# Kernel tuning notes

Measured on AMD Instinct MI355X. Metric: run time of the kernel, lower is better.

Reference implementation:

```python
import jax, jax.numpy as jnp
import numpy as np
import math

B, L, D, H = 4, 1024, 768, 12   # docs, seq_len, hidden, attn heads
E, M, P = 24, 4, 552            # entities/doc, mentions/entity, pairs/doc
EMB, BLK, NL = 768, 64, 97      # emb_size, block_size, num relation labels


def setup_inputs() -> dict:
    key = jax.random.key(0)
    ks = jax.random.split(key, 12)
    s = 0.02  # weight init scale
    return {
        "sequence_output": jax.random.normal(ks[0], (B, L, D), jnp.float32),
        "attention": jax.random.uniform(ks[1], (B, H, L, L), jnp.float32),
        "W_q": jax.random.normal(ks[2], (D, D), jnp.float32) * s,
        "W_k": jax.random.normal(ks[3], (D, D), jnp.float32) * s,
        "head_W": jax.random.normal(ks[4], (2 * D, EMB), jnp.float32) * s,
        "head_b": jax.random.normal(ks[5], (EMB,), jnp.float32) * s,
        "tail_W": jax.random.normal(ks[6], (2 * D, EMB), jnp.float32) * s,
        "tail_b": jax.random.normal(ks[7], (EMB,), jnp.float32) * s,
        "bil_W": jax.random.normal(ks[8], (EMB * BLK, NL), jnp.float32) * s,
        "bil_b": jax.random.normal(ks[9], (NL,), jnp.float32) * s,
        "mention_pos": jax.random.randint(ks[10], (B, E, M), 0, L - 2),
        "hts": jax.random.randint(ks[11], (B, P, 2), 0, E),
    }


def reference(sequence_output, attention, W_q, W_k, head_W, head_b,
              tail_W, tail_b, bil_W, bil_b, mention_pos, hts):
    offset = 1  # bert-style [CLS] offset
    pos = mention_pos + offset                     # [B,E,M] token index of each mention
    bb = jnp.arange(B)[:, None, None]

    # --- mention gathers (padded version of the ragged python loops) ---
    # per-mention attention rows: attention[b, :, pos, :] -> [B,E,M,H,L]
    att_q = attention.transpose(0, 2, 1, 3)        # [B,L,H,L]
    ment_att = att_q[bb, pos]                      # [B,E,M,H,L]
    ent_att = ment_att.mean(axis=2)                # [B,E,H,L]  (mean over mentions)
    # mention embeddings (GAT stage = identity here): [B,E,M,D]
    ment_emb = sequence_output[bb, pos]

    # --- localized context rs via head*tail attention product ---
    bb2 = jnp.arange(B)[:, None]
    h_att = ent_att[bb2, hts[:, :, 0]]             # [B,P,H,L]
    t_att = ent_att[bb2, hts[:, :, 1]]             # [B,P,H,L]
    ht_att = (h_att * t_att).mean(axis=2)          # [B,P,L] (mean over heads)
    ht_att = ht_att / (ht_att.sum(axis=-1, keepdims=True) + 1e-5)
    rs = jnp.einsum('bld,bpl->bpd', sequence_output, ht_att)  # [B,P,D]

    R = B * P
    rs_f = rs.reshape(R, D)

    # --- entity representations via mention-level attention pooling ---
    h_ment = ment_emb[bb2, hts[:, :, 0]].reshape(R, M, D)
    t_ment = ment_emb[bb2, hts[:, :, 1]].reshape(R, M, D)
    q_c = rs_f @ W_q                               # [R,D]
    inv = 1.0 / math.sqrt(D)

    def pool(ment):
        k = ment.reshape(-1, D) @ W_k
        k = k.reshape(R, M, D)
        scores = jnp.einsum('rmd,rd->rm', k, q_c) * inv
        w = jax.nn.softmax(scores, axis=-1)
        return jnp.einsum('rm,rmd->rd', w, ment)

    h_ent = pool(h_ment)                           # [R,D]
    t_ent = pool(t_ment)                           # [R,D]

    # --- extractors + grouped bilinear classifier ---
    hs = jnp.tanh(jnp.concatenate([h_ent, rs_f], axis=1) @ head_W + head_b)
    ts = jnp.tanh(jnp.concatenate([t_ent, rs_f], axis=1) @ tail_W + tail_b)
    K = EMB // BLK
    b1 = hs.reshape(R, K, BLK)
    b2 = ts.reshape(R, K, BLK)
    bl = (b1[:, :, :, None] * b2[:, :, None, :]).reshape(R, EMB * BLK)
    logits = bl @ bil_W + bil_b                    # [R,NL]
    return logits
```

## Files before the change

### kernel.cpp

```cpp
#include <hip/hip_runtime.h>
#include <hip/hip_bf16.h>
#include <math.h>

#define Bc 4
#define Lc 1024
#define Dc 768
#define Hc 12
#define Ec 24
#define Mc 4
#define Pc 552
#define EMBc 768
#define NLc 97
#define Rc (Bc*Pc)
#define KSPL 48
#define HT_ABS (35*32*512)

typedef __attribute__((ext_vector_type(4))) float f32x4;
typedef __attribute__((ext_vector_type(8))) short short8;
typedef __attribute__((ext_vector_type(4))) unsigned short us4;
typedef _Float16 f16x8 __attribute__((ext_vector_type(8)));

static __device__ __forceinline__ unsigned short f2bf(float x){
  unsigned int u = __float_as_uint(x);
  unsigned int r = u + 0x7fffu + ((u >> 16) & 1u);
  return (unsigned short)(r >> 16);
}
static __device__ __forceinline__ unsigned short f2h(float x){
  _Float16 h = (_Float16)x;
  return __builtin_bit_cast(unsigned short, h);
}
static __device__ __forceinline__ float h2f(unsigned short x){
  return (float)__builtin_bit_cast(_Float16, x);
}
static __device__ __forceinline__ size_t flin_off(int r, int kk, int KT){
  return ((size_t)(r>>4)*KT + (kk>>5))*512 + (size_t)((((kk&31)>>3)*16 + (r&15))*8) + (kk&7);
}

__global__ __launch_bounds__(256) void k_prep(const float* __restrict__ bilW, unsigned short* __restrict__ Wbf,
                                              const float* __restrict__ seq, unsigned short* __restrict__ seqf,
                                              const float* __restrict__ W_q, unsigned short* __restrict__ Wq_f,
                                              const float* __restrict__ W_k, unsigned short* __restrict__ Wk_f,
                                              const float* __restrict__ headW, unsigned short* __restrict__ headW_f,
                                              const float* __restrict__ tailW, unsigned short* __restrict__ tailW_f,
                                              const float* __restrict__ att, const int* __restrict__ mpos,
                                              float* __restrict__ ent_att,
                                              unsigned short* __restrict__ ment_bf){
  int bx = blockIdx.x;
  int tid = threadIdx.x;
  __shared__ float t[64][65];
  if (bx < 1536){
    const float* Ws = bilW + (size_t)bx*32*NLc;
    unsigned short* o = Wbf + (size_t)bx*4480;
    float* w = &t[0][0];
    for (int idx = tid; idx < 32*NLc; idx += 256)
      w[idx] = Ws[idx];
    __syncthreads();
    #pragma unroll
    for (int q8 = 0; q8 < 18; q8++){
      int idx = q8*256 + tid;
      if (idx < 4480){
        int n = idx / 40, kk = idx - n*40;
        float v = (kk < 32 && n < NLc) ? w[kk*NLc + n] : 0.f;
        o[idx] = f2h(v);
      }
    }
    return;
  }
  if (bx >= 3168){
    int blk = bx - 3168;
    int h  = blk % Hc;
    int be = blk / Hc;
    int b  = be / Ec;
    int p0 = mpos[be*Mc+0]+1, p1 = mpos[be*Mc+1]+1;
    int p2 = mpos[be*Mc+2]+1, p3 = mpos[be*Mc+3]+1;
    const float* ab = att + ((size_t)b*Hc + h)*Lc*Lc;
    const float* a0 = ab + (size_t)p0*Lc;
    const float* a1 = ab + (size_t)p1*Lc;
    const float* a2 = ab + (size_t)p2*Lc;
    const float* a3 = ab + (size_t)p3*Lc;
    float* o = ent_att + (size_t)blk*Lc;
    int l4 = tid*4;
    float4 v0 = *(const float4*)(a0 + l4);
    float4 v1 = *(const float4*)(a1 + l4);
    float4 v2 = *(const float4*)(a2 + l4);
    float4 v3 = *(const float4*)(a3 + l4);
    float4 ov;
    ov.x = 0.25f*(v0.x+v1.x+v2.x+v3.x);
    ov.y = 0.25f*(v0.y+v1.y+v2.y+v3.y);
    ov.z = 0.25f*(v0.z+v1.z+v2.z+v3.z);
    ov.w = 0.25f*(v0.w+v1.w+v2.w+v3.w);
    *(float4*)(o + l4) = ov;
    int gidx = blk*256 + tid;
    int d = gidx % Dc;
    int bem = gidx / Dc;
    int bb = bem / (Ec*Mc);
    int pos = mpos[bem] + 1;
    float v = seq[((size_t)bb*Lc + pos)*Dc + d];
    ment_bf[flin_off(bem, d, 24)] = f2bf(v);
    return;
  }
  bx -= 1536;
  const float* src; unsigned short* dst; int tk, tn, KTW;
  if (bx < 768){
    int z = bx / 192, rem = bx % 192;
    src = seq + (size_t)z*Lc*Dc; dst = seqf + (size_t)z*(Dc/16)*(Lc/32)*512;
    tk = rem % 16; tn = rem / 16; KTW = 32;
  } else if (bx < 768+144){
    int rem = bx - 768;
    src = W_q; dst = Wq_f; tk = rem % 12; tn = rem / 12; KTW = 24;
  } else if (bx < 768+288){
    int rem = bx - (768+144);
    src = W_k; dst = Wk_f; tk = rem % 12; tn = rem / 12; KTW = 24;
  } else if (bx < 768+288+288){
    int rem = bx - (768+288);
    src = headW; dst = headW_f; tk = rem % 24; tn = rem / 24; KTW = 48;
  } else {
    int rem = bx - (768+288+288);
    src = tailW; dst = tailW_f; tk = rem % 24; tn = rem / 24; KTW = 48;
  }
  int r0 = tk*64, c0 = tn*64;
  #pragma unroll
  for (int q8 = 0; q8 < 16; q8++){
    int idx = q8*256 + tid;
    int rr = idx >> 6, cc = idx & 63;
    t[rr][cc] = src[(size_t)(r0+rr)*768 + c0+cc];
  }
  __syncthreads();
  #pragma unroll
  for (int q8 = 0; q8 < 16; q8++){
    int idx = q8*256 + tid;
    int li = idx & 511, sub = idx >> 9;
    int nt_l = sub >> 1, kt_l = sub & 1;
    int lane = li >> 3, e = li & 7;
    int kl = kt_l*32 + (lane>>4)*8 + e;
    int nl = nt_l*16 + (lane&15);
    dst[ ((size_t)(c0/16 + nt_l)*KTW + (r0/32 + kt_l))*512 + li ] = f2bf(t[kl][nl]);
  }
}

__global__ __launch_bounds__(256) void k_ht_att(const float* __restrict__ ent_att,
                                                const int* __restrict__ hts,
                                                unsigned short* __restrict__ htbf){
  int b = blockIdx.x & 3;
  int p = blockIdx.x >> 2;
  unsigned short* o = htbf + (size_t)b*HT_ABS;
  int l4 = threadIdx.x*4;
  if (p >= Pc){
    us4 z4 = {0,0,0,0};
    *(us4*)(o + flin_off(p, l4, 32)) = z4;
    return;
  }
  int r = b*Pc + p;
  int hi = hts[r*2+0], ti = hts[r*2+1];
  const float* eh = ent_att + (size_t)(b*Ec+hi)*Hc*Lc;
  const float* et = ent_att + (size_t)(b*Ec+ti)*Hc*Lc;
  __shared__ float raw[Lc];
  __shared__ float wsum[4];
  float4 s4 = {0.f,0.f,0.f,0.f};
  #pragma unroll
  for (int h = 0; h < Hc; h++){
    float4 e1 = *(const float4*)&eh[h*Lc + l4];
    float4 e2 = *(const float4*)&et[h*Lc + l4];
    s4.x = fmaf(e1.x,e2.x,s4.x); s4.y = fmaf(e1.y,e2.y,s4.y);
    s4.z = fmaf(e1.z,e2.z,s4.z); s4.w = fmaf(e1.w,e2.w,s4.w);
  }
  s4.x *= (1.0f/Hc); s4.y *= (1.0f/Hc); s4.z *= (1.0f/Hc); s4.w *= (1.0f/Hc);
  *(float4*)&raw[l4] = s4;
  float lsum = s4.x+s4.y+s4.z+s4.w;
  for (int off = 32; off; off >>= 1) lsum += __shfl_down(lsum, off);
  if ((threadIdx.x & 63) == 0) wsum[threadIdx.x>>6] = lsum;
  __syncthreads();
  float inv = 1.0f/(wsum[0]+wsum[1]+wsum[2]+wsum[3] + 1e-5f);
  float4 rv = *(const float4*)&raw[l4];
  us4 v4;
  v4[0] = f2bf(rv.x*inv); v4[1] = f2bf(rv.y*inv);
  v4[2] = f2bf(rv.z*inv); v4[3] = f2bf(rv.w*inv);
  *(us4*)(o + flin_off(p, l4, 32)) = v4;
}

struct FJob {
  const unsigned short* A1; const unsigned short* W; const float* bias; void* C;
  int M; int mtmax; int Wktw; int rowsPerBatch;
  size_t Abs; size_t Wbs;
};
struct FJobs {
  FJob j[6]; int xs[7]; int n;
};

template<int KT1, int CT, int NT>
__global__ __launch_bounds__(256) void k_fgemmN(FJobs P){
  int tid = threadIdx.x;
  int jx = 0;
  for (int tjob = 1; tjob < P.n; tjob++)
    if ((int)blockIdx.x >= P.xs[tjob]) jx = tjob;
  FJob j = P.j[jx];
  int mbx = blockIdx.x - P.xs[jx];
  int z = blockIdx.z;
  int lane = tid & 63, wid = tid >> 6;
  int row16 = lane & 15, oct = lane >> 4;

  __shared__ __align__(16) unsigned short Wlds[NT*KT1*512];
  {
    const unsigned short* wpan = j.W + (size_t)z*j.Wbs + (size_t)(blockIdx.y*NT)*j.Wktw*512;
    constexpr int UNITS = NT*KT1*64;
    #pragma unroll
    for (int it = 0; it < UNITS/256; ++it){
      int u = it*256 + tid;
      int f = u >> 6;
      int n = f / KT1, kt = f - n*KT1;
      size_t so = (((size_t)(n*j.Wktw + kt)) << 9) + (size_t)((u & 63) << 3);
      __builtin_amdgcn_global_load_lds(
          (const __attribute__((address_space(1))) unsigned int*)(wpan + so),
          (__attribute__((address_space(3))) unsigned int*)((char*)Wlds + (size_t)u*16),
          16, 0, 0);
    }
  }

  int rb = mbx*128 + wid*32;
  int mt0 = rb >> 4;       if (mt0 >= j.mtmax) mt0 = j.mtmax - 1;
  int mt1 = (rb >> 4) + 1; if (mt1 >= j.mtmax) mt1 = j.mtmax - 1;
  const unsigned short* ap0 = j.A1 + (size_t)z*j.Abs + (size_t)mt0*KT1*512 + lane*8;
  const unsigned short* ap1 = j.A1 + (size_t)z*j.Abs + (size_t)mt1*KT1*512 + lane*8;
  f32x4 acc[2][NT];
  #pragma unroll
  for (int m = 0; m < 2; m++)
    #pragma unroll
    for (int n = 0; n < NT; n++) acc[m][n] = (f32x4){0.f,0.f,0.f,0.f};

  __syncthreads();

  #pragma unroll 4
  for (int kt = 0; kt < KT1; kt++){
    short8 a0 = *(const short8*)(ap0 + (size_t)kt*512);
    short8 a1 = *(const short8*)(ap1 + (size_t)kt*512);
    #pragma unroll
    for (int n = 0; n < NT; n++){
      short8 bv = *(const short8*)&Wlds[(n*KT1 + kt)*512 + lane*8];
      acc[0][n] = __builtin_amdgcn_mfma_f32_16x16x32_bf16(a0, bv, acc[0][n], 0, 0, 0);
      acc[1][n] = __builtin_amdgcn_mfma_f32_16x16x32_bf16(a1, bv, acc[1][n], 0, 0, 0);
    }
  }
  int colb = blockIdx.y*(NT*16);
  #pragma unroll
  for (int m = 0; m < 2; m++)
    #pragma unroll
    for (int n = 0; n < NT; n++)
      #pragma unroll
      for (int jj = 0; jj < 4; jj++){
        int r = rb + m*16 + oct*4 + jj;
        if (r < j.M){
          int col = colb + n*16 + row16;
          float v = acc[m][n][jj];
          if (CT == 0 && j.bias) v += j.bias[col];
          int rg = z*j.rowsPerBatch + r;
          if (CT == 2){
            ((unsigned short*)j.C)[flin_off(rg, col, 24)] = f2bf(v);
          } else {
            ((float*)j.C)[(size_t)rg*768 + col] = v;
          }
        }
      }
}

__global__ __launch_bounds__(256) void k_pool(const float* __restrict__ kment,
                                              const float* __restrict__ q_c,
                                              const float* __restrict__ rsWh,
                                              const float* __restrict__ rsWt,
                                              const float* __restrict__ mWh,
                                              const float* __restrict__ mWt,
                                              const float* __restrict__ headb,
                                              const float* __restrict__ tailb,
                                              const int* __restrict__ hts,
                                              unsigned short* __restrict__ hs16,
                                              unsigned short* __restrict__ ts16){
  int wid = threadIdx.x >> 6, lane = threadIdx.x & 63;
  int r = blockIdx.x*4 + wid;
  int b = r / Pc;
  float q[12];
  const float* qp = q_c + (size_t)r*Dc + lane;
  #pragma unroll
  for (int u = 0; u < 12; u++) q[u] = qp[u*64];
  const float invs = 0.03608439182435161f;
  #pragma unroll
  for (int side = 0; side < 2; side++){
    int e = hts[r*2+side];
    const float* kb = kment + (size_t)(b*Ec+e)*Mc*Dc + lane;
    float part[Mc] = {0.f,0.f,0.f,0.f};
    #pragma unroll
    for (int m = 0; m < Mc; m++)
      #pragma unroll
      for (int u = 0; u < 12; u++)
        part[m] = fmaf(kb[m*Dc + u*64], q[u], part[m]);
    #pragma unroll
    for (int m = 0; m < Mc; m++)
      #pragma unroll
      for (int off = 1; off < 64; off <<= 1)
        part[m] += __shfl_xor(part[m], off);
    float mx = fmaxf(fmaxf(part[0],part[1]), fmaxf(part[2],part[3])) * invs;
    float w0 = expf(part[0]*invs - mx), w1 = expf(part[1]*invs - mx);
    float w2 = expf(part[2]*invs - mx), w3 = expf(part[3]*invs - mx);
    float isum = 1.0f/(w0+w1+w2+w3);
    w0 *= isum; w1 *= isum; w2 *= isum; w3 *= isum;
    const float* mW  = (side ? mWt  : mWh) + (size_t)(b*Ec+e)*Mc*Dc;
    const float* rsW = (side ? rsWt : rsWh) + (size_t)r*Dc;
    const float* bias = side ? tailb : headb;
    unsigned short* o = (side ? ts16 : hs16) + (size_t)r*Dc;
    #pragma unroll
    for (int u = 0; u < 12; u++){
      int d = lane + u*64;
      float v = rsW[d] + bias[d]
              + w0*mW[d] + w1*mW[Dc+d] + w2*mW[2*Dc+d] + w3*mW[3*Dc+d];
      o[d] = f2h(tanhf(v));
    }
  }
}

__global__ __launch_bounds__(256) void k_bilinear_mfma(
    const unsigned short* __restrict__ hs16, const unsigned short* __restrict__ ts16,
    const unsigned short* __restrict__ Wbf,
    unsigned short* __restrict__ partial)
{
  int mb = blockIdx.x / KSPL;
  int kb = blockIdx.x % KSPL;
  int k  = kb >> 2;
  int i0 = (kb & 3) * 16;

  int tid  = threadIdx.x;
  int lane = tid & 63;
  int wid  = tid >> 6;
  int row16 = lane & 15;
  int oct   = lane >> 4;

  int rbase = mb*256 + wid*64;

  __shared__ __align__(16) unsigned short Wlds[2][8960];

  f16x8 tsh[4][2];
  f16x8 hsh[4][2];
  #pragma unroll
  for (int m = 0; m < 4; m++){
    int r = rbase + m*16 + row16; if (r > Rc-1) r = Rc-1;
    const unsigned short* tp = ts16 + (size_t)r*EMBc + k*64;
    tsh[m][0] = __builtin_bit_cast(f16x8, *(const short8*)(tp + oct*8));
    tsh[m][1] = __builtin_bit_cast(f16x8, *(const short8*)(tp + 32 + oct*8));
    const unsigned short* hp = hs16 + (size_t)r*EMBc + k*64 + i0;
    hsh[m][0] = __builtin_bit_cast(f16x8, *(const short8*)(hp));
    hsh[m][1] = __builtin_bit_cast(f16x8, *(const short8*)(hp + 8));
  }

  const char* wsrc = (const char*)(Wbf + ((size_t)(k*128 + i0*2))*4480);

  #pragma unroll
  for (int rr = 0; rr < 5; rr++){
    int u = tid + rr*256;
    if (u < 1120)
      __builtin_amdgcn_global_load_lds(
        (const __attribute__((address_space(1))) unsigned int*)(wsrc + (size_t)u*16),
        (__attribute__((address_space(3))) unsigned int*)((char*)&Wlds[0][0] + u*16),
        16, 0, 0);
  }

  f32x4 acc[4][7];
  #pragma unroll
  for (int m = 0; m < 4; m++)
    #pragma unroll
    for (int n = 0; n < 7; n++) acc[m][n] = (f32x4){0.f,0.f,0.f,0.f};

  __syncthreads();

  #pragma unroll
  for (int cp = 0; cp < 16; cp++){
    int cur = cp & 1;
    if (cp < 15){
      const char* nsrc = wsrc + (size_t)(cp+1)*17920;
      #pragma unroll
      for (int rr = 0; rr < 5; rr++){
        int u = tid + rr*256;
        if (u < 1120)
          __builtin_amdgcn_global_load_lds(
            (const __attribute__((address_space(1))) unsigned int*)(nsrc + (size_t)u*16),
            (__attribute__((address_space(3))) unsigned int*)((char*)&Wlds[cur^1][0] + u*16),
            16, 0, 0);
      }
    }
    #pragma unroll
    for (int half = 0; half < 2; half++){
      f16x8 af[4];
      #pragma unroll
      for (int m = 0; m < 4; m++){
        _Float16 hv = hsh[m][cp>>3][cp&7];
        f16x8 hvb = {hv,hv,hv,hv,hv,hv,hv,hv};
        af[m] = tsh[m][half] * hvb;
      }
      #pragma unroll
      for (int n = 0; n < 7; n++){
        f16x8 bfr = __builtin_bit_cast(f16x8,
            *(const short8*)&Wlds[cur][half*4480 + (n*16 + row16)*40 + oct*8]);
        #pragma unroll
        for (int m = 0; m < 4; m++)
          acc[m][n] = __builtin_amdgcn_mfma_f32_16x16x32_f16(af[m], bfr, acc[m][n], 0, 0, 0);
      }
    }
    __syncthreads();
  }

  unsigned short* pk = partial + (size_t)kb*Rc*NLc;
  #pragma unroll
  for (int m = 0; m < 4; m++){
    #pragma unroll
    for (int n = 0; n < 7; n++){
      #pragma unroll
      for (int j = 0; j < 4; j++){
        int r = rbase + m*16 + oct*4 + j;
        int col = n*16 + row16;
        if (r < Rc && col < NLc)
          pk[(size_t)r*NLc + col] = f2h(acc[m][n][j]);
      }
    }
  }
}

__global__ __launch_bounds__(256) void k_reduce(const unsigned short* __restrict__ partial,
                                                const float* __restrict__ bilb,
                                                float* __restrict__ out){
  int idx = blockIdx.x*256 + threadIdx.x;
  if (idx >= Rc*NLc) return;
  int n = idx % NLc;
  float s = bilb[n];
  #pragma unroll
  for (int ks = 0; ks < KSPL; ks++) s += h2f(partial[(size_t)ks*Rc*NLc + idx]);
  out[idx] = s;
}

extern "C" void kernel_launch(void* const* d_in, const int* in_sizes, int n_in,
                              void* d_out, int out_size, void* d_ws, size_t ws_size,
                              hipStream_t stream){
  const float* seq   = (const float*)d_in[0];
  const float* att   = (const float*)d_in[1];
  const float* W_q   = (const float*)d_in[2];
  const float* W_k   = (const float*)d_in[3];
  const float* headW = (const float*)d_in[4];
  const float* headb = (const float*)d_in[5];
  const float* tailW = (const float*)d_in[6];
  const float* tailb = (const float*)d_in[7];
  const float* bilW  = (const float*)d_in[8];
  const float* bilb  = (const float*)d_in[9];
  const int*   mpos  = (const int*)d_in[10];
  const int*   hts   = (const int*)d_in[11];
  float* out = (float*)d_out;

  float* ws = (float*)d_ws;
  float* ent_att = ws;
  float* q_c     = ws + 1179648;
  float* kment   = q_c + 1695744;
  float* ment_unused = kment + 294912;
  unsigned short* seqf    = (unsigned short*)(ment_unused + 294912);
  unsigned short* htbf    = seqf + 3145728;
  unsigned short* rs_bf   = htbf + 4*HT_ABS;
  unsigned short* ment_bf = rs_bf + 1695744;
  unsigned short* Wq_f    = ment_bf + 294912;
  unsigned short* Wk_f    = Wq_f + 589824;
  unsigned short* headW_f = Wk_f + 589824;
  unsigned short* tailW_f = headW_f + 1179648;
  unsigned short* hs16 = tailW_f + 1179648;
  unsigned short* ts16 = hs16 + 1695744;
  unsigned short* Wbf  = ts16 + 1695744;
  float* rsWh = (float*)(Wbf + 6881280);
  float* rsWt = rsWh + 1695744;
  float* mWh  = rsWt + 1695744;
  float* mWt  = mWh + 294912;
  unsigned short* partial = (unsigned short*)ws;

  k_prep   <<<4320, 256, 0, stream>>>(bilW, Wbf, seq, seqf, W_q, Wq_f, W_k, Wk_f,
                                      headW, headW_f, tailW, tailW_f,
                                      att, mpos, ent_att, ment_bf);
  k_ht_att <<<4*560, 256, 0, stream>>>(ent_att, hts, htbf);
  {
    FJobs P{};
    P.j[0] = { htbf, seqf, nullptr, rs_bf, Pc, 35, 32, Pc,
               (size_t)HT_ABS, (size_t)(48*32*512) };
    P.xs[0] = 0; P.xs[1] = 5; P.n = 1;
    k_fgemmN<32,2,2><<<dim3(5,24,4), 256, 0, stream>>>(P);
  }
  {
    FJobs P{};
    P.j[0] = { rs_bf,   Wq_f,              nullptr, q_c,   Rc,  138, 24, 0, 0, 0 };
    P.j[1] = { ment_bf, Wk_f,              nullptr, kment, 384,  24, 24, 0, 0, 0 };
    P.j[2] = { rs_bf,   headW_f + 24*512,  nullptr, rsWh,  Rc,  138, 48, 0, 0, 0 };
    P.j[3] = { rs_bf,   tailW_f + 24*512,  nullptr, rsWt,  Rc,  138, 48, 0, 0, 0 };
    P.j[4] = { ment_bf, headW_f,           nullptr, mWh,   384,  24, 48, 0, 0, 0 };
    P.j[5] = { ment_bf, tailW_f,           nullptr, mWt,   384,  24, 48, 0, 0, 0 };
    P.xs[0]=0; P.xs[1]=18; P.xs[2]=21; P.xs[3]=39; P.xs[4]=57; P.xs[5]=60; P.xs[6]=63;
    P.n = 6;
    k_fgemmN<24,0,2><<<dim3(63,24), 256, 0, stream>>>(P);
  }
  k_pool   <<<Rc/4, 256, 0, stream>>>(kment, q_c, rsWh, rsWt, mWh, mWt,
                                      headb, tailb, hts, hs16, ts16);
  k_bilinear_mfma<<<9*KSPL, 256, 0, stream>>>(hs16, ts16, Wbf, partial);
  k_reduce <<<(Rc*NLc+255)/256, 256, 0, stream>>>(partial, bilb, out);
}
```

Baseline: 130.4 us.

## Store projection GEMM outputs as fp16 and widen N-tile with K-chunked LDS

The multi-job projection GEMM now writes q, k, rs and mention projections as fp16 rather than fp32 (new CT==3 epilogue). k_pool reads these halves and converts them back to float. The GEMM template gains a K-chunk parameter so the weight panel is staged into LDS in chunks, which allows NT=4 with half as many column blocks. This is meant to cut intermediate memory traffic and redundant A-tile loads, at the cost of fp16 rounding in the intermediates and an extra barrier per chunk.

```diff
diff --git a/kernel.cpp b/kernel.cpp
--- a/kernel.cpp
+++ b/kernel.cpp
@@ -187,7 +187,7 @@
   FJob j[6]; int xs[7]; int n;
 };
 
-template<int KT1, int CT, int NT>
+template<int KT1, int CT, int NT, int KCH>
 __global__ __launch_bounds__(256) void k_fgemmN(FJobs P){
   int tid = threadIdx.x;
   int jx = 0;
@@ -199,22 +199,8 @@
   int lane = tid & 63, wid = tid >> 6;
   int row16 = lane & 15, oct = lane >> 4;
 
-  __shared__ __align__(16) unsigned short Wlds[NT*KT1*512];
-  {
-    const unsigned short* wpan = j.W + (size_t)z*j.Wbs + (size_t)(blockIdx.y*NT)*j.Wktw*512;
-    constexpr int UNITS = NT*KT1*64;
-    #pragma unroll
-    for (int it = 0; it < UNITS/256; ++it){
-      int u = it*256 + tid;
-      int f = u >> 6;
-      int n = f / KT1, kt = f - n*KT1;
-      size_t so = (((size_t)(n*j.Wktw + kt)) << 9) + (size_t)((u & 63) << 3);
-      __builtin_amdgcn_global_load_lds(
-          (const __attribute__((address_space(1))) unsigned int*)(wpan + so),
-          (__attribute__((address_space(3))) unsigned int*)((char*)Wlds + (size_t)u*16),
-          16, 0, 0);
-    }
-  }
+  __shared__ __align__(16) unsigned short Wlds[NT*KCH*512];
+  const unsigned short* wpan = j.W + (size_t)z*j.Wbs + (size_t)(blockIdx.y*NT)*j.Wktw*512;
 
   int rb = mbx*128 + wid*32;
   int mt0 = rb >> 4;       if (mt0 >= j.mtmax) mt0 = j.mtmax - 1;
@@ -227,19 +213,38 @@
     #pragma unroll
     for (int n = 0; n < NT; n++) acc[m][n] = (f32x4){0.f,0.f,0.f,0.f};
 
-  __syncthreads();
-
-  #pragma unroll 4
-  for (int kt = 0; kt < KT1; kt++){
-    short8 a0 = *(const short8*)(ap0 + (size_t)kt*512);
-    short8 a1 = *(const short8*)(ap1 + (size_t)kt*512);
-    #pragma unroll
-    for (int n = 0; n < NT; n++){
-      short8 bv = *(const short8*)&Wlds[(n*KT1 + kt)*512 + lane*8];
-      acc[0][n] = __builtin_amdgcn_mfma_f32_16x16x32_bf16(a0, bv, acc[0][n], 0, 0, 0);
-      acc[1][n] = __builtin_amdgcn_mfma_f32_16x16x32_bf16(a1, bv, acc[1][n], 0, 0, 0);
-    }
-  }
+  #pragma unroll
+  for (int kc = 0; kc < KT1/KCH; kc++){
+    {
+      constexpr int UNITS = NT*KCH*64;
+      #pragma unroll
+      for (int it = 0; it < UNITS/256; ++it){
+        int u = it*256 + tid;
+        int f = u >> 6;
+        int n = f / KCH, kt = f - n*KCH;
+        size_t so = (((size_t)(n*j.Wktw + kc*KCH + kt)) << 9) + (size_t)((u & 63) << 3);
+        __builtin_amdgcn_global_load_lds(
+            (const __attribute__((address_space(1))) unsigned int*)(wpan + so),
+            (__attribute__((address_space(3))) unsigned int*)((char*)Wlds + (size_t)u*16),
+            16, 0, 0);
+      }
+    }
+    __syncthreads();
+    #pragma unroll 4
+    for (int k2 = 0; k2 < KCH; k2++){
+      int kt = kc*KCH + k2;
+      short8 a0 = *(const short8*)(ap0 + (size_t)kt*512);
+      short8 a1 = *(const short8*)(ap1 + (size_t)kt*512);
+      #pragma unroll
+      for (int n = 0; n < NT; n++){
+        short8 bv = *(const short8*)&Wlds[(n*KCH + k2)*512 + lane*8];
+        acc[0][n] = __builtin_amdgcn_mfma_f32_16x16x32_bf16(a0, bv, acc[0][n], 0, 0, 0);
+        acc[1][n] = __builtin_amdgcn_mfma_f32_16x16x32_bf16(a1, bv, acc[1][n], 0, 0, 0);
+      }
+    }
+    if (kc + 1 < KT1/KCH) __syncthreads();
+  }
+
   int colb = blockIdx.y*(NT*16);
   #pragma unroll
   for (int m = 0; m < 2; m++)
@@ -255,6 +260,8 @@
           int rg = z*j.rowsPerBatch + r;
           if (CT == 2){
             ((unsigned short*)j.C)[flin_off(rg, col, 24)] = f2bf(v);
+          } else if (CT == 3){
+            ((unsigned short*)j.C)[(size_t)rg*768 + col] = f2h(v);
           } else {
             ((float*)j.C)[(size_t)rg*768 + col] = v;
           }
@@ -262,12 +269,12 @@
       }
 }
 
-__global__ __launch_bounds__(256) void k_pool(const float* __restrict__ kment,
-                                              const float* __restrict__ q_c,
-                                              const float* __restrict__ rsWh,
-                                              const float* __restrict__ rsWt,
-                                              const float* __restrict__ mWh,
-                                              const float* __restrict__ mWt,
+__global__ __launch_bounds__(256) void k_pool(const unsigned short* __restrict__ km16,
+                                              const unsigned short* __restrict__ q16,
+                                              const unsigned short* __restrict__ rsWh16,
+                                              const unsigned short* __restrict__ rsWt16,
+                                              const unsigned short* __restrict__ mWh16,
+                                              const unsigned short* __restrict__ mWt16,
                                               const float* __restrict__ headb,
                                               const float* __restrict__ tailb,
                                               const int* __restrict__ hts,
@@ -277,20 +284,20 @@
   int r = blockIdx.x*4 + wid;
   int b = r / Pc;
   float q[12];
-  const float* qp = q_c + (size_t)r*Dc + lane;
-  #pragma unroll
-  for (int u = 0; u < 12; u++) q[u] = qp[u*64];
+  const unsigned short* qp = q16 + (size_t)r*Dc + lane;
+  #pragma unroll
+  for (int u = 0; u < 12; u++) q[u] = h2f(qp[u*64]);
   const float invs = 0.03608439182435161f;
   #pragma unroll
   for (int side = 0; side < 2; side++){
     int e = hts[r*2+side];
-    const float* kb = kment + (size_t)(b*Ec+e)*Mc*Dc + lane;
+    const unsigned short* kb = km16 + (size_t)(b*Ec+e)*Mc*Dc + lane;
     float part[Mc] = {0.f,0.f,0.f,0.f};
     #pragma unroll
     for (int m = 0; m < Mc; m++)
       #pragma unroll
       for (int u = 0; u < 12; u++)
-        part[m] = fmaf(kb[m*Dc + u*64], q[u], part[m]);
+        part[m] = fmaf(h2f(kb[m*Dc + u*64]), q[u], part[m]);
     #pragma unroll
     for (int m = 0; m < Mc; m++)
       #pragma unroll
@@ -301,15 +308,15 @@
     float w2 = expf(part[2]*invs - mx), w3 = expf(part[3]*invs - mx);
     float isum = 1.0f/(w0+w1+w2+w3);
     w0 *= isum; w1 *= isum; w2 *= isum; w3 *= isum;
-    const float* mW  = (side ? mWt  : mWh) + (size_t)(b*Ec+e)*Mc*Dc;
-    const float* rsW = (side ? rsWt : rsWh) + (size_t)r*Dc;
+    const unsigned short* mW  = (side ? mWt16  : mWh16) + (size_t)(b*Ec+e)*Mc*Dc;
+    const unsigned short* rsW = (side ? rsWt16 : rsWh16) + (size_t)r*Dc;
     const float* bias = side ? tailb : headb;
     unsigned short* o = (side ? ts16 : hs16) + (size_t)r*Dc;
     #pragma unroll
     for (int u = 0; u < 12; u++){
       int d = lane + u*64;
-      float v = rsW[d] + bias[d]
-              + w0*mW[d] + w1*mW[Dc+d] + w2*mW[2*Dc+d] + w3*mW[3*Dc+d];
+      float v = h2f(rsW[d]) + bias[d]
+              + w0*h2f(mW[d]) + w1*h2f(mW[Dc+d]) + w2*h2f(mW[2*Dc+d]) + w3*h2f(mW[3*Dc+d]);
       o[d] = f2h(tanhf(v));
     }
   }
@@ -451,10 +458,10 @@
 
   float* ws = (float*)d_ws;
   float* ent_att = ws;
-  float* q_c     = ws + 1179648;
-  float* kment   = q_c + 1695744;
-  float* ment_unused = kment + 294912;
-  unsigned short* seqf    = (unsigned short*)(ment_unused + 294912);
+  unsigned short* base = (unsigned short*)(ws + 1179648);
+  unsigned short* q16     = base;
+  unsigned short* km16    = q16 + 1695744;
+  unsigned short* seqf    = km16 + 294912;
   unsigned short* htbf    = seqf + 3145728;
   unsigned short* rs_bf   = htbf + 4*HT_ABS;
   unsigned short* ment_bf = rs_bf + 1695744;
@@ -462,13 +469,13 @@
   unsigned short* Wk_f    = Wq_f + 589824;
   unsigned short* headW_f = Wk_f + 589824;
   unsigned short* tailW_f = headW_f + 1179648;
-  unsigned short* hs16 = tailW_f + 1179648;
-  unsigned short* ts16 = hs16 + 1695744;
-  unsigned short* Wbf  = ts16 + 1695744;
-  float* rsWh = (float*)(Wbf + 6881280);
-  float* rsWt = rsWh + 1695744;
-  float* mWh  = rsWt + 1695744;
-  float* mWt  = mWh + 294912;
+  unsigned short* hs16    = tailW_f + 1179648;
+  unsigned short* ts16    = hs16 + 1695744;
+  unsigned short* Wbf     = ts16 + 1695744;
+  unsigned short* rsWh16  = Wbf + 6881280;
+  unsigned short* rsWt16  = rsWh16 + 1695744;
+  unsigned short* mWh16   = rsWt16 + 1695744;
+  unsigned short* mWt16   = mWh16 + 294912;
   unsigned short* partial = (unsigned short*)ws;
 
   k_prep   <<<4320, 256, 0, stream>>>(bilW, Wbf, seq, seqf, W_q, Wq_f, W_k, Wk_f,
@@ -480,21 +487,21 @@
     P.j[0] = { htbf, seqf, nullptr, rs_bf, Pc, 35, 32, Pc,
                (size_t)HT_ABS, (size_t)(48*32*512) };
     P.xs[0] = 0; P.xs[1] = 5; P.n = 1;
-    k_fgemmN<32,2,2><<<dim3(5,24,4), 256, 0, stream>>>(P);
+    k_fgemmN<32,2,2,32><<<dim3(5,24,4), 256, 0, stream>>>(P);
   }
   {
     FJobs P{};
-    P.j[0] = { rs_bf,   Wq_f,              nullptr, q_c,   Rc,  138, 24, 0, 0, 0 };
-    P.j[1] = { ment_bf, Wk_f,              nullptr, kment, 384,  24, 24, 0, 0, 0 };
-    P.j[2] = { rs_bf,   headW_f + 24*512,  nullptr, rsWh,  Rc,  138, 48, 0, 0, 0 };
-    P.j[3] = { rs_bf,   tailW_f + 24*512,  nullptr, rsWt,  Rc,  138, 48, 0, 0, 0 };
-    P.j[4] = { ment_bf, headW_f,           nullptr, mWh,   384,  24, 48, 0, 0, 0 };
-    P.j[5] = { ment_bf, tailW_f,           nullptr, mWt,   384,  24, 48, 0, 0, 0 };
+    P.j[0] = { rs_bf,   Wq_f,              nullptr, q16,    Rc,  138, 24, 0, 0, 0 };
+    P.j[1] = { ment_bf, Wk_f,              nullptr, km16,   384,  24, 24, 0, 0, 0 };
+    P.j[2] = { rs_bf,   headW_f + 24*512,  nullptr, rsWh16, Rc,  138, 48, 0, 0, 0 };
+    P.j[3] = { rs_bf,   tailW_f + 24*512,  nullptr, rsWt16, Rc,  138, 48, 0, 0, 0 };
+    P.j[4] = { ment_bf, headW_f,           nullptr, mWh16,  384,  24, 48, 0, 0, 0 };
+    P.j[5] = { ment_bf, tailW_f,           nullptr, mWt16,  384,  24, 48, 0, 0, 0 };
     P.xs[0]=0; P.xs[1]=18; P.xs[2]=21; P.xs[3]=39; P.xs[4]=57; P.xs[5]=60; P.xs[6]=63;
     P.n = 6;
-    k_fgemmN<24,0,2><<<dim3(63,24), 256, 0, stream>>>(P);
-  }
-  k_pool   <<<Rc/4, 256, 0, stream>>>(kment, q_c, rsWh, rsWt, mWh, mWt,
+    k_fgemmN<24,3,4,12><<<dim3(63,12), 256, 0, stream>>>(P);
+  }
+  k_pool   <<<Rc/4, 256, 0, stream>>>(km16, q16, rsWh16, rsWt16, mWh16, mWt16,
                                       headb, tailb, hts, hs16, ts16);
   k_bilinear_mfma<<<9*KSPL, 256, 0, stream>>>(hs16, ts16, Wbf, partial);
   k_reduce <<<(Rc*NLc+255)/256, 256, 0, stream>>>(partial, bilb, out);
```

Measured after the change: 122.3 us. 6.2% less time.
